# Performance work log

Hardware: AMD Instinct MI355X
Metric: run time of the kernel (lower is better)

## Reference

```python
import jax, jax.numpy as jnp
import numpy as np

B, T, D = 4, 8192, 1024
C = 8.0


def setup_inputs() -> dict:
    key = jax.random.key(0)
    k1, k2, k3 = jax.random.split(key, 3)
    init_std = D ** (-0.5)
    x = jax.random.normal(k1, (B, T, D), dtype=jnp.float32)
    W_in = jax.random.truncated_normal(k2, -3.0, 3.0, (D, D), dtype=jnp.float32) * init_std
    W_gate = jax.random.truncated_normal(k3, -3.0, 3.0, (D, D), dtype=jnp.float32) * init_std
    b_in = jnp.zeros((D,), dtype=jnp.float32)
    b_gate = jnp.zeros((D,), dtype=jnp.float32)
    forget_lambda = jnp.linspace(-4.323, -9.0, D, dtype=jnp.float32)
    return {"x": x, "W_in": W_in, "b_in": b_in, "W_gate": W_gate,
            "b_gate": b_gate, "forget_lambda": forget_lambda}


def _combine(c1, c2):
    # linear recurrence h_t = a_t * h_{t-1} + b_t  (associative composition)
    a1, b1 = c1
    a2, b2 = c2
    return a1 * a2, a2 * b1 + b2


def reference(x, W_in, b_in, W_gate, b_gate, forget_lambda):
    # x: [B, T, D]
    input_gate = x @ W_in.T + b_in          # [B, T, D]
    recurrence_gate = x @ W_gate.T + b_gate  # [B, T, D]
    alpha = jnp.exp(-C * jax.nn.softplus(forget_lambda) * jax.nn.sigmoid(recurrence_gate))
    beta = jnp.sqrt(1.0 - alpha ** 2 + 1e-6)
    xbeta = beta * jax.nn.sigmoid(input_gate) * x
    # parallel scan of h_t = alpha_t * h_{t-1} + xbeta_t along sequence axis
    _, h = jax.lax.associative_scan(_combine, (alpha, xbeta), axis=1)
    return h
```

## Files before the change

kernel.cpp:

```cpp
#include <hip/hip_runtime.h>

typedef unsigned short u16;
typedef __attribute__((ext_vector_type(8))) short short8;
typedef __attribute__((ext_vector_type(4))) float f32x4;

#define T_SEQ 8192
#define DDIM 1024
#define BB 4
#define MM (BB * T_SEQ)
#define NC 128
#define CHUNK (T_SEQ / NC)
#define CHAINS (BB * DDIM)
#define NHT 32

__device__ __forceinline__ float bf_lo(unsigned p) {
    union { unsigned u; float f; } v; v.u = p << 16; return v.f;
}
__device__ __forceinline__ float bf_hi(unsigned p) {
    union { unsigned u; float f; } v; v.u = p & 0xffff0000u; return v.f;
}
__device__ __forceinline__ float bf_u16(u16 p) {
    union { unsigned u; float f; } v; v.u = ((unsigned)p) << 16; return v.f;
}
__device__ __forceinline__ u16 f2bf(float f) {
    union { unsigned u; float f; } v; v.f = f;
    unsigned r = v.u + 0x7fffu + ((v.u >> 16) & 1u);
    return (u16)(r >> 16);
}
__device__ __forceinline__ float sigm(float z) {
    return __builtin_amdgcn_rcpf(1.0f + __expf(-z));
}
__device__ __forceinline__ void gld16(const u16* g, u16* l) {
    __builtin_amdgcn_global_load_lds((const __attribute__((address_space(1))) void*)g,
                                     (__attribute__((address_space(3))) void*)l, 16, 0, 0);
}

#define N4X (MM * DDIM / 4)
#define N4W (DDIM * DDIM / 4)
__global__ __launch_bounds__(256) void cvt_all(const float* __restrict__ x,
                                               const float* __restrict__ Wi,
                                               const float* __restrict__ Wg,
                                               u16* __restrict__ Xb,
                                               u16* __restrict__ Wib,
                                               u16* __restrict__ Wgb) {
    int i = blockIdx.x * 256 + threadIdx.x;
    const float* src; u16* dst; int j;
    if (i < N4X)            { src = x;  dst = Xb;  j = i; }
    else if (i < N4X + N4W) { src = Wi; dst = Wib; j = i - N4X; }
    else                    { src = Wg; dst = Wgb; j = i - N4X - N4W; }
    float4 v = ((const float4*)src)[j];
    ushort4 o;
    o.x = f2bf(v.x); o.y = f2bf(v.y); o.z = f2bf(v.z); o.w = f2bf(v.w);
    ((ushort4*)dst)[j] = o;
}


#define MROW(i_, av)                                                                   \
    acc[i_][0] = __builtin_amdgcn_mfma_f32_16x16x32_bf16(av, b0, acc[i_][0], 0, 0, 0); \
    acc[i_][1] = __builtin_amdgcn_mfma_f32_16x16x32_bf16(av, b1, acc[i_][1], 0, 0, 0); \
    acc[i_][2] = __builtin_amdgcn_mfma_f32_16x16x32_bf16(av, b2, acc[i_][2], 0, 0, 0); \
    acc[i_][3] = __builtin_amdgcn_mfma_f32_16x16x32_bf16(av, b3, acc[i_][3], 0, 0, 0);

#define LDA_S(s_, i) (*(const short8*)&lds[(s_)*8192 + (arow0 + (i)*16)*32 + aoff])
#define LDB_S(s_, j) (*(const short8*)&lds[32768 + (s_)*8192 + (brow0 + (j)*16)*32 + aoff])

#define STA_S(ds_, ht_, rb) gld16(gA + (size_t)(ht_)*32 + (size_t)(rb)*128*DDIM,       \
                                  &lds[(ds_)*8192 + (rb)*4096 + tid*8])
#define STB_S(ds_, ht_, hf) gld16(((hf) ? gBg : gBi) + (size_t)(ht_)*32,               \
                                  &lds[32768 + (ds_)*8192 + (hf)*4096 + tid*8])

#define PHASE_A(s_, ds_, ht_, DOST)                                                    \
    b0 = LDB_S(s_, 0); b1 = LDB_S(s_, 1); b2 = LDB_S(s_, 2); b3 = LDB_S(s_, 3);        \
    a0 = LDA_S(s_, 0); a1 = LDA_S(s_, 1); a2 = LDA_S(s_, 2); a3 = LDA_S(s_, 3);        \
    if (DOST) { STA_S(ds_, ht_, 0); STA_S(ds_, ht_, 1); }                              \
    __builtin_amdgcn_s_barrier();                                                      \
    asm volatile("s_waitcnt lgkmcnt(0)" ::: "memory");                                 \
    __builtin_amdgcn_sched_barrier(0);                                                 \
    __builtin_amdgcn_s_setprio(1);                                                     \
    MROW(0, a0) MROW(1, a1) MROW(2, a2) MROW(3, a3)                                    \
    __builtin_amdgcn_s_setprio(0);                                                     \
    __builtin_amdgcn_s_barrier();

#define PHASE_B(s_, ds_, ht_, DOST, VMS)                                               \
    a0 = LDA_S(s_, 4); a1 = LDA_S(s_, 5); a2 = LDA_S(s_, 6); a3 = LDA_S(s_, 7);        \
    if (DOST) { STB_S(ds_, ht_, 0); STB_S(ds_, ht_, 1); }                              \
    asm volatile("s_waitcnt " VMS ::: "memory");                                       \
    __builtin_amdgcn_s_barrier();                                                      \
    asm volatile("s_waitcnt lgkmcnt(0)" ::: "memory");                                 \
    __builtin_amdgcn_sched_barrier(0);                                                 \
    __builtin_amdgcn_s_setprio(1);                                                     \
    MROW(4, a0) MROW(5, a1) MROW(6, a2) MROW(7, a3)                                    \
    __builtin_amdgcn_s_setprio(0);                                                     \
    __builtin_amdgcn_s_barrier();

#define PAIR(s_, ds_, ht_, DOST, VMS)                                                  \
    PHASE_A(s_, ds_, ht_, DOST)                                                        \
    PHASE_B(s_, ds_, ht_, DOST, VMS)

__global__ __launch_bounds__(512, 2)
void gemm_fused(const u16* __restrict__ X, const u16* __restrict__ Wi,
                const u16* __restrict__ Wg, const float* __restrict__ b_in,
                const float* __restrict__ b_gate, const float* __restrict__ lam,
                u16* __restrict__ Sg, u16* __restrict__ XBg) {
    const int bid = blockIdx.x;
    const int xcd = bid & 7;
    const int r = bid >> 3;
    const int n_tile = r & 7;
    const int m_tile = xcd * 16 + (r >> 3);
    const int tN0 = n_tile * 128;
    const int tM0 = m_tile * 256;

    const int tid = threadIdx.x;
    const int lane = tid & 63;
    const int w = tid >> 6;
    const int wm = w >> 2;
    const int wn = w & 3;
    const int gate = wn >> 1;
    const int wn_sub = wn & 1;

    __shared__ u16 lds[65536];

    const int srow = tid >> 2;
    const int c8log = (tid & 3) ^ ((tid >> 3) & 3);
    const u16* gA  = X  + (size_t)(tM0 + srow) * DDIM + c8log * 8;
    const u16* gBi = Wi + (size_t)(tN0 + srow) * DDIM + c8log * 8;
    const u16* gBg = Wg + (size_t)(tN0 + srow) * DDIM + c8log * 8;

    const int lm = lane & 15;
    const int aoff = (((lane >> 4) ^ ((lm >> 1) & 3))) * 8;
    const int arow0 = wm * 128 + lm;
    const int brow0 = gate * 128 + wn_sub * 64 + lm;

    f32x4 acc[8][4] = {};
    short8 a0, a1, a2, a3, b0, b1, b2, b3;

    STA_S(0, 0, 0); STA_S(0, 0, 1); STB_S(0, 0, 0); STB_S(0, 0, 1);
    STA_S(1, 1, 0); STA_S(1, 1, 1); STB_S(1, 1, 0); STB_S(1, 1, 1);
    STA_S(2, 2, 0); STA_S(2, 2, 1); STB_S(2, 2, 0); STB_S(2, 2, 1);
    asm volatile("s_waitcnt vmcnt(8)" ::: "memory");
    __builtin_amdgcn_s_barrier();

    for (int g = 0; g < 7; ++g) {
        const int hb = 4 * g;
        PAIR(0, 3, hb + 3, 1, "vmcnt(8)")
        PAIR(1, 0, hb + 4, 1, "vmcnt(8)")
        PAIR(2, 1, hb + 5, 1, "vmcnt(8)")
        PAIR(3, 2, hb + 6, 1, "vmcnt(8)")
    }
    PAIR(0, 3, 31, 1, "vmcnt(8)")
    PAIR(1, 0, 0, 0, "vmcnt(4)")
    PAIR(2, 0, 0, 0, "vmcnt(0)")
    PAIR(3, 0, 0, 0, "vmcnt(0)")

    const int r0 = (lane >> 4) << 2;
    const int cb = lane & 15;
    if (gate) {
#pragma unroll
        for (int j = 0; j < 4; ++j) {
            const int colg = tN0 + wn_sub * 64 + j * 16 + cb;
            const int cl = wn_sub * 64 + j * 16 + cb;
            const float bj = b_gate[colg];
            const float nsp = -8.0f * log1pf(__expf(lam[colg]));
#pragma unroll
            for (int i = 0; i < 8; ++i) {
                const int rl0 = wm * 128 + i * 16 + r0;
#pragma unroll
                for (int rr = 0; rr < 4; ++rr) {
                    const int rl = rl0 + rr;
                    float s = nsp * sigm(acc[i][j][rr] + bj);
                    lds[rl * 128 + (cl ^ (((rl >> 2) & 7) << 4))] = f2bf(s);
                }
            }
        }
    } else {
#pragma unroll
        for (int j = 0; j < 4; ++j) {
            const int colg = tN0 + wn_sub * 64 + j * 16 + cb;
            const int cl = wn_sub * 64 + j * 16 + cb;
            const float bj = b_in[colg];
#pragma unroll
            for (int i = 0; i < 8; ++i) {
                const int rl0 = wm * 128 + i * 16 + r0;
#pragma unroll
                for (int rr = 0; rr < 4; ++rr) {
                    const int rl = rl0 + rr;
                    float p = sigm(acc[i][j][rr] + bj);
                    lds[32768 + rl * 128 + (cl ^ (((rl >> 2) & 7) << 4))] =
                        (u16)(p * 65535.0f + 0.5f);
                }
            }
        }
    }
    asm volatile("s_waitcnt lgkmcnt(0)" ::: "memory");
    __builtin_amdgcn_s_barrier();
    __builtin_amdgcn_sched_barrier(0);

    const int cc = tid & 15;
    const int rg0 = (tid >> 4) * 8;
#pragma unroll
    for (int k = 0; k < 8; ++k) {
        const int rl = rg0 + k;
        const int ch = (cc ^ (((rl >> 2) & 7) << 1)) * 8;
        short8 sv = *(const short8*)&lds[rl * 128 + ch];
        short8 pv = *(const short8*)&lds[32768 + rl * 128 + ch];
        const size_t go = (size_t)(tM0 + rl) * DDIM + tN0 + cc * 8;
        short8 xv = *(const short8*)&X[go];
        short8 ov;
#pragma unroll
        for (int e = 0; e < 8; ++e) {
            float s = bf_u16((u16)sv[e]);
            float p = (float)((u16)pv[e]) * (1.0f / 65535.0f);
            float xf = bf_u16((u16)xv[e]);
            float be = sqrtf(1.0f - __expf(2.0f * s) + 1e-6f);
            ov[e] = (short)f2bf(be * p * xf);
        }
        *(short8*)&Sg[go] = sv;
        *(short8*)&XBg[go] = ov;
    }
}

__global__ __launch_bounds__(256)
void scan_pass1(const u16* __restrict__ S, const u16* __restrict__ XB,
                float* __restrict__ AggA, float* __restrict__ AggB) {
    const int c = blockIdx.x, dblk = blockIdx.y, bq = blockIdx.z;
    const int d0 = dblk * 512 + threadIdx.x * 2;
    size_t base = ((size_t)(bq * T_SEQ + c * CHUNK)) * DDIM + d0;

    float A0 = 1.0f, B0 = 0.0f, A1 = 1.0f, B1 = 0.0f;
#pragma unroll 8
    for (int t = 0; t < CHUNK; t++) {
        unsigned sp = *(const unsigned*)(S + base);
        unsigned xp = *(const unsigned*)(XB + base);
        float a0 = __expf(bf_lo(sp));
        float a1 = __expf(bf_hi(sp));
        B0 = fmaf(a0, B0, bf_lo(xp)); A0 *= a0;
        B1 = fmaf(a1, B1, bf_hi(xp)); A1 *= a1;
        base += DDIM;
    }
    const int chain = bq * DDIM + d0;
    float2 av; av.x = A0; av.y = A1;
    float2 bv; bv.x = B0; bv.y = B1;
    *(float2*)(AggA + (size_t)c * CHAINS + chain) = av;
    *(float2*)(AggB + (size_t)c * CHAINS + chain) = bv;
}

__global__ __launch_bounds__(256)
void scan_pass2(const float* __restrict__ AggA, const float* __restrict__ AggB,
                float* __restrict__ H0) {
    const int chain = blockIdx.x * 256 + threadIdx.x;
    float p = 0.0f;
#pragma unroll 8
    for (int c = 0; c < NC; c++) {
        H0[(size_t)c * CHAINS + chain] = p;
        p = AggA[(size_t)c * CHAINS + chain] * p + AggB[(size_t)c * CHAINS + chain];
    }
}

__global__ __launch_bounds__(256)
void scan_pass3(const u16* __restrict__ S, const u16* __restrict__ XB,
                const float* __restrict__ H0, float* __restrict__ out) {
    const int c = blockIdx.x, dblk = blockIdx.y, bq = blockIdx.z;
    const int d0 = dblk * 512 + threadIdx.x * 2;
    size_t base = ((size_t)(bq * T_SEQ + c * CHUNK)) * DDIM + d0;
    const int chain = bq * DDIM + d0;

    float2 h = *(const float2*)(H0 + (size_t)c * CHAINS + chain);
#pragma unroll 8
    for (int t = 0; t < CHUNK; t++) {
        unsigned sp = *(const unsigned*)(S + base);
        unsigned xp = *(const unsigned*)(XB + base);
        float a0 = __expf(bf_lo(sp));
        float a1 = __expf(bf_hi(sp));
        h.x = fmaf(a0, h.x, bf_lo(xp));
        h.y = fmaf(a1, h.y, bf_hi(xp));
        *(float2*)(out + base) = h;
        base += DDIM;
    }
}

extern "C" void kernel_launch(void* const* d_in, const int* in_sizes, int n_in,
                              void* d_out, int out_size, void* d_ws, size_t ws_size,
                              hipStream_t stream) {
    const float* x   = (const float*)d_in[0];
    const float* Win = (const float*)d_in[1];
    const float* bin = (const float*)d_in[2];
    const float* Wg  = (const float*)d_in[3];
    const float* bg  = (const float*)d_in[4];
    const float* lam = (const float*)d_in[5];
    float* out = (float*)d_out;

    char* w = (char*)d_ws;
    u16* Wi_bf  = (u16*)(w);
    u16* Wg_bf  = (u16*)(w + (size_t)(2) * 1024 * 1024);
    u16* Sg     = (u16*)(w + (size_t)(4) * 1024 * 1024);
    u16* XBg    = (u16*)(w + (size_t)(68) * 1024 * 1024);
    float* AggA = (float*)(w + (size_t)(132) * 1024 * 1024);
    float* AggB = (float*)(w + (size_t)(134) * 1024 * 1024);
    float* H0   = (float*)(w + (size_t)(136) * 1024 * 1024);

    u16* Xbf = (u16*)d_out;

    cvt_all<<<dim3((N4X + 2 * N4W) / 256), dim3(256), 0, stream>>>(
        x, Win, Wg, Xbf, Wi_bf, Wg_bf);

    gemm_fused<<<dim3((DDIM / 128) * (MM / 256)), dim3(512), 0, stream>>>(
        Xbf, Wi_bf, Wg_bf, bin, bg, lam, Sg, XBg);

    scan_pass1<<<dim3(NC, 2, BB), dim3(256), 0, stream>>>(Sg, XBg, AggA, AggB);
    scan_pass2<<<dim3(CHAINS / 256), dim3(256), 0, stream>>>(AggA, AggB, H0);
    scan_pass3<<<dim3(NC, 2, BB), dim3(256), 0, stream>>>(Sg, XBg, H0, out);
}
```

Measured before the change: 467.0 us.

## Software-pipeline LDS fragment reads with double-buffered registers in GEMM main loop

Restructures the GEMM k-loop so the LDS reads for the next k-slice (B fragments and first half of A) are issued right after the barrier and overlap with the MFMAs of the current slice, using double-buffered register sets. The two barriers per half-step and the explicit lgkmcnt waits/sched_barriers are replaced by a single barrier per k-step. This aims to hide LDS latency and cut barrier overhead, at the cost of more VGPRs held live (up to 16 short8 fragments), which could pressure the 2-block occupancy target. It relies on the compiler to insert correct lgkmcnt waits.

```diff
diff --git a/kernel.cpp b/kernel.cpp
--- a/kernel.cpp
+++ b/kernel.cpp
@@ -55,47 +55,43 @@
 }
 
 
-#define MROW(i_, av)                                                                   \
-    acc[i_][0] = __builtin_amdgcn_mfma_f32_16x16x32_bf16(av, b0, acc[i_][0], 0, 0, 0); \
-    acc[i_][1] = __builtin_amdgcn_mfma_f32_16x16x32_bf16(av, b1, acc[i_][1], 0, 0, 0); \
-    acc[i_][2] = __builtin_amdgcn_mfma_f32_16x16x32_bf16(av, b2, acc[i_][2], 0, 0, 0); \
-    acc[i_][3] = __builtin_amdgcn_mfma_f32_16x16x32_bf16(av, b3, acc[i_][3], 0, 0, 0);
+#define MROW4(ri, af, bf)                                                               \
+    acc[ri][0] = __builtin_amdgcn_mfma_f32_16x16x32_bf16(af, bf[0], acc[ri][0], 0,0,0); \
+    acc[ri][1] = __builtin_amdgcn_mfma_f32_16x16x32_bf16(af, bf[1], acc[ri][1], 0,0,0); \
+    acc[ri][2] = __builtin_amdgcn_mfma_f32_16x16x32_bf16(af, bf[2], acc[ri][2], 0,0,0); \
+    acc[ri][3] = __builtin_amdgcn_mfma_f32_16x16x32_bf16(af, bf[3], acc[ri][3], 0,0,0);
+
+#define MQUAD(b_, aset, bset) MROW4((b_)+0, aset[0], bset) MROW4((b_)+1, aset[1], bset) \
+                              MROW4((b_)+2, aset[2], bset) MROW4((b_)+3, aset[3], bset)
 
 #define LDA_S(s_, i) (*(const short8*)&lds[(s_)*8192 + (arow0 + (i)*16)*32 + aoff])
 #define LDB_S(s_, j) (*(const short8*)&lds[32768 + (s_)*8192 + (brow0 + (j)*16)*32 + aoff])
+
+#define RD_A(dst, s_, base) { dst[0] = LDA_S(s_, (base)+0); dst[1] = LDA_S(s_, (base)+1); \
+                              dst[2] = LDA_S(s_, (base)+2); dst[3] = LDA_S(s_, (base)+3); }
+#define RD_B(dst, s_)       { dst[0] = LDB_S(s_, 0); dst[1] = LDB_S(s_, 1);               \
+                              dst[2] = LDB_S(s_, 2); dst[3] = LDB_S(s_, 3); }
 
 #define STA_S(ds_, ht_, rb) gld16(gA + (size_t)(ht_)*32 + (size_t)(rb)*128*DDIM,       \
                                   &lds[(ds_)*8192 + (rb)*4096 + tid*8])
 #define STB_S(ds_, ht_, hf) gld16(((hf) ? gBg : gBi) + (size_t)(ht_)*32,               \
                                   &lds[32768 + (ds_)*8192 + (hf)*4096 + tid*8])
 
-#define PHASE_A(s_, ds_, ht_, DOST)                                                    \
-    b0 = LDB_S(s_, 0); b1 = LDB_S(s_, 1); b2 = LDB_S(s_, 2); b3 = LDB_S(s_, 3);        \
-    a0 = LDA_S(s_, 0); a1 = LDA_S(s_, 1); a2 = LDA_S(s_, 2); a3 = LDA_S(s_, 3);        \
-    if (DOST) { STA_S(ds_, ht_, 0); STA_S(ds_, ht_, 1); }                              \
+#define PAIR_(s_, sn_, ds_, ht_, BCUR, BNXT, DOST, VMS, DORD)                          \
+               \
+    RD_A(A1, s_, 4)                                                                    \
+    __builtin_amdgcn_s_setprio(1);                                                     \
+    MQUAD(0, A0, BCUR)                                                                 \
+    __builtin_amdgcn_s_setprio(0);                                                     \
+    asm volatile("s_waitcnt " VMS ::: "memory");                 \
     __builtin_amdgcn_s_barrier();                                                      \
-    asm volatile("s_waitcnt lgkmcnt(0)" ::: "memory");                                 \
-    __builtin_amdgcn_sched_barrier(0);                                                 \
+                  \
+    if (DORD) { RD_B(BNXT, sn_) RD_A(A0, sn_, 0) }                                     \
+    if (DOST) { STA_S(ds_, ht_, 0); STA_S(ds_, ht_, 1);                                \
+                STB_S(ds_, ht_, 0); STB_S(ds_, ht_, 1); }                              \
     __builtin_amdgcn_s_setprio(1);                                                     \
-    MROW(0, a0) MROW(1, a1) MROW(2, a2) MROW(3, a3)                                    \
-    __builtin_amdgcn_s_setprio(0);                                                     \
-    __builtin_amdgcn_s_barrier();
-
-#define PHASE_B(s_, ds_, ht_, DOST, VMS)                                               \
-    a0 = LDA_S(s_, 4); a1 = LDA_S(s_, 5); a2 = LDA_S(s_, 6); a3 = LDA_S(s_, 7);        \
-    if (DOST) { STB_S(ds_, ht_, 0); STB_S(ds_, ht_, 1); }                              \
-    asm volatile("s_waitcnt " VMS ::: "memory");                                       \
-    __builtin_amdgcn_s_barrier();                                                      \
-    asm volatile("s_waitcnt lgkmcnt(0)" ::: "memory");                                 \
-    __builtin_amdgcn_sched_barrier(0);                                                 \
-    __builtin_amdgcn_s_setprio(1);                                                     \
-    MROW(4, a0) MROW(5, a1) MROW(6, a2) MROW(7, a3)                                    \
-    __builtin_amdgcn_s_setprio(0);                                                     \
-    __builtin_amdgcn_s_barrier();
-
-#define PAIR(s_, ds_, ht_, DOST, VMS)                                                  \
-    PHASE_A(s_, ds_, ht_, DOST)                                                        \
-    PHASE_B(s_, ds_, ht_, DOST, VMS)
+    MQUAD(4, A1, BCUR)                                                                 \
+    __builtin_amdgcn_s_setprio(0);
 
 __global__ __launch_bounds__(512, 2)
 void gemm_fused(const u16* __restrict__ X, const u16* __restrict__ Wi,
@@ -132,25 +128,28 @@
     const int brow0 = gate * 128 + wn_sub * 64 + lm;
 
     f32x4 acc[8][4] = {};
-    short8 a0, a1, a2, a3, b0, b1, b2, b3;
+    short8 A0[4], A1[4], B0[4], B1[4];
 
     STA_S(0, 0, 0); STA_S(0, 0, 1); STB_S(0, 0, 0); STB_S(0, 0, 1);
     STA_S(1, 1, 0); STA_S(1, 1, 1); STB_S(1, 1, 0); STB_S(1, 1, 1);
     STA_S(2, 2, 0); STA_S(2, 2, 1); STB_S(2, 2, 0); STB_S(2, 2, 1);
     asm volatile("s_waitcnt vmcnt(8)" ::: "memory");
     __builtin_amdgcn_s_barrier();
+    RD_B(B0, 0) RD_A(A0, 0, 0)
 
     for (int g = 0; g < 7; ++g) {
         const int hb = 4 * g;
-        PAIR(0, 3, hb + 3, 1, "vmcnt(8)")
-        PAIR(1, 0, hb + 4, 1, "vmcnt(8)")
-        PAIR(2, 1, hb + 5, 1, "vmcnt(8)")
-        PAIR(3, 2, hb + 6, 1, "vmcnt(8)")
-    }
-    PAIR(0, 3, 31, 1, "vmcnt(8)")
-    PAIR(1, 0, 0, 0, "vmcnt(4)")
-    PAIR(2, 0, 0, 0, "vmcnt(0)")
-    PAIR(3, 0, 0, 0, "vmcnt(0)")
+        PAIR_(0, 1, 3, hb + 3, B0, B1, 1, "vmcnt(4)", 1)
+        PAIR_(1, 2, 0, hb + 4, B1, B0, 1, "vmcnt(4)", 1)
+        PAIR_(2, 3, 1, hb + 5, B0, B1, 1, "vmcnt(4)", 1)
+        PAIR_(3, 0, 2, hb + 6, B1, B0, 1, "vmcnt(4)", 1)
+    }
+    PAIR_(0, 1, 3, 31, B0, B1, 1, "vmcnt(4)", 1)
+    PAIR_(1, 2, 0, 0,  B1, B0, 0, "vmcnt(4)", 1)
+    PAIR_(2, 3, 0, 0,  B0, B1, 0, "vmcnt(0)", 1)
+    PAIR_(3, 0, 0, 0,  B1, B0, 0, "vmcnt(0)", 0)
+    asm volatile("s_waitcnt lgkmcnt(0)" ::: "memory");
+    __builtin_amdgcn_s_barrier();
 
     const int r0 = (lane >> 4) << 2;
     const int cb = lane & 15;
```

New measurement: 470.8 us. About the same (+0.8%).

## Fuse chunk-aggregate scan pass into GEMM epilogue and widen pass-3 vectors

Applied to the files above, without the earlier changes.

Computes the per-chunk (A,B) scan aggregates inside the GEMM epilogue, using each thread's 8 rows and then an LDS reduction across 8 segments per 64-row chunk. This removes the scan_pass1 kernel and its full re-read of S and XB from global memory. Pass 3 now handles 4 channels per thread with ushort4/float4 accesses, so one block covers all 1024 columns. The epilogue grows longer and adds LDS traffic and barriers, and the aggregates are built from the rounded bf16 xbeta values so they stay consistent with pass 3.

```diff
diff --git a/kernel.cpp b/kernel.cpp
--- a/kernel.cpp
+++ b/kernel.cpp
@@ -11,7 +11,6 @@
 #define NC 128
 #define CHUNK (T_SEQ / NC)
 #define CHAINS (BB * DDIM)
-#define NHT 32
 
 __device__ __forceinline__ float bf_lo(unsigned p) {
     union { unsigned u; float f; } v; v.u = p << 16; return v.f;
@@ -101,7 +100,8 @@
 void gemm_fused(const u16* __restrict__ X, const u16* __restrict__ Wi,
                 const u16* __restrict__ Wg, const float* __restrict__ b_in,
                 const float* __restrict__ b_gate, const float* __restrict__ lam,
-                u16* __restrict__ Sg, u16* __restrict__ XBg) {
+                u16* __restrict__ Sg, u16* __restrict__ XBg,
+                float* __restrict__ AggA, float* __restrict__ AggB) {
     const int bid = blockIdx.x;
     const int xcd = bid & 7;
     const int r = bid >> 3;
@@ -197,6 +197,8 @@
 
     const int cc = tid & 15;
     const int rg0 = (tid >> 4) * 8;
+    float Aacc[8] = {1.f, 1.f, 1.f, 1.f, 1.f, 1.f, 1.f, 1.f};
+    float Bacc[8] = {};
 #pragma unroll
     for (int k = 0; k < 8; ++k) {
         const int rl = rg0 + k;
@@ -212,36 +214,45 @@
             float p = (float)((u16)pv[e]) * (1.0f / 65535.0f);
             float xf = bf_u16((u16)xv[e]);
             float be = sqrtf(1.0f - __expf(2.0f * s) + 1e-6f);
-            ov[e] = (short)f2bf(be * p * xf);
+            u16 xbq = f2bf(be * p * xf);
+            ov[e] = (short)xbq;
+            float a = __expf(s);
+            Bacc[e] = fmaf(a, Bacc[e], bf_u16(xbq));
+            Aacc[e] *= a;
         }
         *(short8*)&Sg[go] = sv;
         *(short8*)&XBg[go] = ov;
     }
-}
-
-__global__ __launch_bounds__(256)
-void scan_pass1(const u16* __restrict__ S, const u16* __restrict__ XB,
-                float* __restrict__ AggA, float* __restrict__ AggB) {
-    const int c = blockIdx.x, dblk = blockIdx.y, bq = blockIdx.z;
-    const int d0 = dblk * 512 + threadIdx.x * 2;
-    size_t base = ((size_t)(bq * T_SEQ + c * CHUNK)) * DDIM + d0;
-
-    float A0 = 1.0f, B0 = 0.0f, A1 = 1.0f, B1 = 0.0f;
-#pragma unroll 8
-    for (int t = 0; t < CHUNK; t++) {
-        unsigned sp = *(const unsigned*)(S + base);
-        unsigned xp = *(const unsigned*)(XB + base);
-        float a0 = __expf(bf_lo(sp));
-        float a1 = __expf(bf_hi(sp));
-        B0 = fmaf(a0, B0, bf_lo(xp)); A0 *= a0;
-        B1 = fmaf(a1, B1, bf_hi(xp)); A1 *= a1;
-        base += DDIM;
-    }
-    const int chain = bq * DDIM + d0;
-    float2 av; av.x = A0; av.y = A1;
-    float2 bv; bv.x = B0; bv.y = B1;
-    *(float2*)(AggA + (size_t)c * CHAINS + chain) = av;
-    *(float2*)(AggB + (size_t)c * CHAINS + chain) = bv;
+
+    asm volatile("s_waitcnt lgkmcnt(0)" ::: "memory");
+    __builtin_amdgcn_s_barrier();
+    {
+        float* fA = (float*)lds;
+        float* fB = (float*)lds + 4096;
+        const int seg = tid >> 4;
+#pragma unroll
+        for (int e = 0; e < 8; ++e) {
+            fA[seg * 128 + cc * 8 + e] = Aacc[e];
+            fB[seg * 128 + cc * 8 + e] = Bacc[e];
+        }
+        asm volatile("s_waitcnt lgkmcnt(0)" ::: "memory");
+        __builtin_amdgcn_s_barrier();
+        const int chk = tid >> 7;
+        const int col = tid & 127;
+        float A = 1.0f, Bv = 0.0f;
+#pragma unroll
+        for (int k = 0; k < 8; ++k) {
+            float a = fA[(chk * 8 + k) * 128 + col];
+            float b = fB[(chk * 8 + k) * 128 + col];
+            Bv = fmaf(a, Bv, b);
+            A *= a;
+        }
+        const int bq = tM0 >> 13;
+        const int cw = ((tM0 & 8191) >> 6) + chk;
+        const size_t gi = (size_t)cw * CHAINS + bq * DDIM + tN0 + col;
+        AggA[gi] = A;
+        AggB[gi] = Bv;
+    }
 }
 
 __global__ __launch_bounds__(256)
@@ -259,21 +270,21 @@
 __global__ __launch_bounds__(256)
 void scan_pass3(const u16* __restrict__ S, const u16* __restrict__ XB,
                 const float* __restrict__ H0, float* __restrict__ out) {
-    const int c = blockIdx.x, dblk = blockIdx.y, bq = blockIdx.z;
-    const int d0 = dblk * 512 + threadIdx.x * 2;
+    const int c = blockIdx.x, bq = blockIdx.z;
+    const int d0 = threadIdx.x * 4;
     size_t base = ((size_t)(bq * T_SEQ + c * CHUNK)) * DDIM + d0;
     const int chain = bq * DDIM + d0;
 
-    float2 h = *(const float2*)(H0 + (size_t)c * CHAINS + chain);
-#pragma unroll 8
+    float4 h = *(const float4*)(H0 + (size_t)c * CHAINS + chain);
+#pragma unroll 4
     for (int t = 0; t < CHUNK; t++) {
-        unsigned sp = *(const unsigned*)(S + base);
-        unsigned xp = *(const unsigned*)(XB + base);
-        float a0 = __expf(bf_lo(sp));
-        float a1 = __expf(bf_hi(sp));
-        h.x = fmaf(a0, h.x, bf_lo(xp));
-        h.y = fmaf(a1, h.y, bf_hi(xp));
-        *(float2*)(out + base) = h;
+        ushort4 sp = *(const ushort4*)(S + base);
+        ushort4 xp = *(const ushort4*)(XB + base);
+        h.x = fmaf(__expf(bf_u16(sp.x)), h.x, bf_u16(xp.x));
+        h.y = fmaf(__expf(bf_u16(sp.y)), h.y, bf_u16(xp.y));
+        h.z = fmaf(__expf(bf_u16(sp.z)), h.z, bf_u16(xp.z));
+        h.w = fmaf(__expf(bf_u16(sp.w)), h.w, bf_u16(xp.w));
+        *(float4*)(out + base) = h;
         base += DDIM;
     }
 }
@@ -304,9 +315,8 @@
         x, Win, Wg, Xbf, Wi_bf, Wg_bf);
 
     gemm_fused<<<dim3((DDIM / 128) * (MM / 256)), dim3(512), 0, stream>>>(
-        Xbf, Wi_bf, Wg_bf, bin, bg, lam, Sg, XBg);
-
-    scan_pass1<<<dim3(NC, 2, BB), dim3(256), 0, stream>>>(Sg, XBg, AggA, AggB);
+        Xbf, Wi_bf, Wg_bf, bin, bg, lam, Sg, XBg, AggA, AggB);
+
     scan_pass2<<<dim3(CHAINS / 256), dim3(256), 0, stream>>>(AggA, AggB, H0);
-    scan_pass3<<<dim3(NC, 2, BB), dim3(256), 0, stream>>>(Sg, XBg, H0, out);
-}
+    scan_pass3<<<dim3(NC, 1, BB), dim3(256), 0, stream>>>(Sg, XBg, H0, out);
+}
```

Result: no change. 461.5 us (-1.2%).
